# Optimization experiments

Hardware: AMD Instinct MI355X
Metric: run time of the kernel (lower is better)

Reference implementation:

```python
import jax, jax.numpy as jnp
import numpy as np


def setup_inputs() -> dict:
    key = jax.random.key(0)
    B, L, D, N = 2, 2048, 1024, 16
    ks = jax.random.split(key, 8)
    s = 1.0 / np.sqrt(D)
    # S4D-real init for A_log, matching the module
    A_log = jnp.log(jnp.broadcast_to(jnp.arange(1, N + 1, dtype=jnp.float32), (D, N)))
    return {
        "x": jax.random.normal(ks[0], (B, L, D), jnp.float32),
        "Wz": jax.random.normal(ks[1], (D, D), jnp.float32) * s,
        "bz": jnp.zeros((D,), jnp.float32),
        "Wx": jax.random.normal(ks[2], (D, D), jnp.float32) * s,
        "bx": jnp.zeros((D,), jnp.float32),
        "WB": jax.random.normal(ks[3], (D, N), jnp.float32) * s,
        "bB": jnp.zeros((N,), jnp.float32),
        "WC": jax.random.normal(ks[4], (D, N), jnp.float32) * s,
        "bC": jnp.zeros((N,), jnp.float32),
        "Wdt": jax.random.normal(ks[5], (D, D), jnp.float32) * s,
        "bdt": jnp.zeros((D,), jnp.float32),
        "A_log": A_log,
        "Wout": jax.random.normal(ks[6], (D, D), jnp.float32) * s,
        "bout": jnp.zeros((D,), jnp.float32),
    }


def reference(x, Wz, bz, Wx, bx, WB, bB, WC, bC, Wdt, bdt, A_log, Wout, bout):
    B, L, D = x.shape
    N = A_log.shape[1]

    # input-dependent projections
    z = jax.nn.sigmoid(x @ Wz + bz)            # (B,L,D) gate
    x_ssm = x @ Wx + bx                        # (B,L,D)
    Bm = x @ WB + bB                           # (B,L,N)
    C = x @ WC + bC                            # (B,L,N)
    dt = jax.nn.softplus(x @ Wdt + bdt)        # (B,L,D)

    A = -jnp.exp(A_log)                        # (D,N)
    A_bar = jnp.exp(dt[..., None] * A)         # (B,L,D,N) discretized state matrix
    # x_db = x_ssm * (dt * B)  -> (B,L,D,N)
    x_db = x_ssm[..., None] * (dt[..., None] * Bm[..., None, :])

    # scan over time: move L to leading axis
    a_scan = jnp.transpose(A_bar, (1, 0, 2, 3))   # (L,B,D,N)
    x_scan = jnp.transpose(x_db, (1, 0, 2, 3))    # (L,B,D,N)
    c_scan = jnp.transpose(C, (1, 0, 2))          # (L,B,N)

    def ssm_step(h, inp):
        a_t, x_t, c_t = inp                       # (B,D,N),(B,D,N),(B,N)
        h_new = a_t * h + x_t
        y_t = jnp.einsum('bdn,bn->bd', h_new, c_t)
        return h_new, y_t

    h0 = jnp.zeros((B, D, N), x.dtype)
    _, y_ssm = jax.lax.scan(ssm_step, h0, (a_scan, x_scan, c_scan))
    y_ssm = jnp.transpose(y_ssm, (1, 0, 2))       # (B,L,D)

    y = y_ssm * z
    return y @ Wout + bout
```

## Files before the change

### kernel.cpp

```cpp
#include <hip/hip_runtime.h>
#include <math.h>

#define CHUNKS 64
#define LCH    32

#define GBM 128
#define GBN 128
#define GBK 32
#define ATILE (GBM * GBK)
#define BTILE (GBN * GBK)

typedef __attribute__((ext_vector_type(8))) short bf16x8;
typedef __attribute__((ext_vector_type(4))) float f32x4;
typedef __attribute__((ext_vector_type(8))) unsigned short us8;
typedef __attribute__((ext_vector_type(4))) unsigned short us4;

typedef __attribute__((address_space(1))) const unsigned int gu32;
typedef __attribute__((address_space(3))) unsigned int lu32;

__device__ __forceinline__ void gload16(const unsigned short* g, unsigned short* l) {
    __builtin_amdgcn_global_load_lds((gu32*)g, (lu32*)l, 16, 0, 0);
}

__device__ __forceinline__ unsigned short f2bf(float f) {
    unsigned int u = __float_as_uint(f);
    unsigned int r = (u + 0x7FFFu + ((u >> 16) & 1u)) >> 16;
    return (unsigned short)r;
}
__device__ __forceinline__ float bf2f(unsigned short u) {
    return __uint_as_float((unsigned)u << 16);
}

__global__ __launch_bounds__(256) void transpose4_bf16(
    const float* __restrict__ W0, const float* __restrict__ W1,
    const float* __restrict__ W2, const float* __restrict__ W3,
    unsigned short* __restrict__ T0, unsigned short* __restrict__ T1,
    unsigned short* __restrict__ T2, unsigned short* __restrict__ T3, int D)
{
    const float* W = (blockIdx.z == 0) ? W0 : (blockIdx.z == 1) ? W1
                   : (blockIdx.z == 2) ? W2 : W3;
    unsigned short* Wt = (blockIdx.z == 0) ? T0 : (blockIdx.z == 1) ? T1
                       : (blockIdx.z == 2) ? T2 : T3;

    __shared__ float Ls[64][65];
    const int n0 = blockIdx.x * 64;
    const int k0 = blockIdx.y * 64;
    const int tx = threadIdx.x;

#pragma unroll
    for (int i = 0; i < 4; i++) {
        int idx = tx + i * 256;
        int kr = idx >> 4;
        int ng = idx & 15;
        float4 v = *(const float4*)&W[(size_t)(k0 + kr) * D + n0 + ng * 4];
        Ls[kr][ng * 4 + 0] = v.x;
        Ls[kr][ng * 4 + 1] = v.y;
        Ls[kr][ng * 4 + 2] = v.z;
        Ls[kr][ng * 4 + 3] = v.w;
    }
    __syncthreads();
#pragma unroll
    for (int i = 0; i < 4; i++) {
        int idx = tx + i * 256;
        int nr = idx >> 4;
        int kg = idx & 15;
        us4 u;
#pragma unroll
        for (int j = 0; j < 4; j++) u[j] = f2bf(Ls[kg * 4 + j][nr]);
        *(us4*)&Wt[(size_t)(n0 + nr) * D + k0 + kg * 4] = u;
    }
}

__device__ __forceinline__ void stage_tile(
    const unsigned short* __restrict__ A, const unsigned short* __restrict__ B,
    unsigned short* As, unsigned short* Bs,
    int brow, int bcol, int K, int k0, int wave, int srow, int sq)
{
    gload16(&A[(size_t)(brow + wave * 32      + srow) * K + k0 + sq],
            &As[(wave * 32) * GBK]);
    gload16(&A[(size_t)(brow + wave * 32 + 16 + srow) * K + k0 + sq],
            &As[(wave * 32 + 16) * GBK]);
    gload16(&B[(size_t)(bcol + wave * 32      + srow) * K + k0 + sq],
            &Bs[(wave * 32) * GBK]);
    gload16(&B[(size_t)(bcol + wave * 32 + 16 + srow) * K + k0 + sq],
            &Bs[(wave * 32 + 16) * GBK]);
}

__device__ __forceinline__ void gemm_core(
    const unsigned short* __restrict__ A, const unsigned short* __restrict__ B,
    unsigned short* As, unsigned short* Bs,
    int brow, int bcol, int K, f32x4 acc[4][4],
    int wave, int lane, int wr, int wc, int lrow, int lk)
{
    const int srow = lane >> 2;
    const int sq   = ((lane & 3) ^ ((lane >> 3) & 3)) * 8;

#pragma unroll
    for (int m = 0; m < 4; m++)
#pragma unroll
        for (int n = 0; n < 4; n++) acc[m][n] = (f32x4)(0.f);

    const int nk = K / GBK;
    stage_tile(A, B, As,         Bs,         brow, bcol, K, 0,   wave, srow, sq);
    stage_tile(A, B, As + ATILE, Bs + BTILE, brow, bcol, K, GBK, wave, srow, sq);

    int cur = 0;
    int nxt = 2;
    for (int kt = 0; kt < nk; ++kt) {
        if (kt + 2 < nk) {
            stage_tile(A, B, As + nxt * ATILE, Bs + nxt * BTILE,
                       brow, bcol, K, (kt + 2) * GBK, wave, srow, sq);
            asm volatile("s_waitcnt vmcnt(8)" ::: "memory");
        } else if (kt + 1 < nk) {
            asm volatile("s_waitcnt vmcnt(4)" ::: "memory");
        } else {
            asm volatile("s_waitcnt vmcnt(0)" ::: "memory");
        }
        __builtin_amdgcn_s_barrier();

        const unsigned short* as = As + cur * ATILE;
        const unsigned short* bs = Bs + cur * BTILE;

        bf16x8 av[4], bv[4];
#pragma unroll
        for (int m = 0; m < 4; m++) {
            int row = wr * 64 + m * 16 + lrow;
            av[m] = *(const bf16x8*)&as[row * GBK + ((lk ^ ((row >> 1) & 3)) * 8)];
        }
#pragma unroll
        for (int n = 0; n < 4; n++) {
            int row = wc * 64 + n * 16 + lrow;
            bv[n] = *(const bf16x8*)&bs[row * GBK + ((lk ^ ((row >> 1) & 3)) * 8)];
        }
#pragma unroll
        for (int m = 0; m < 4; m++)
#pragma unroll
            for (int n = 0; n < 4; n++)
                acc[m][n] = __builtin_amdgcn_mfma_f32_16x16x32_bf16(
                    av[m], bv[n], acc[m][n], 0, 0, 0);

        asm volatile("s_waitcnt lgkmcnt(0)" ::: "memory");
        __builtin_amdgcn_s_barrier();
        cur = (cur == 2) ? 0 : cur + 1;
        nxt = (nxt == 2) ? 0 : nxt + 1;
    }
}

__global__ __launch_bounds__(256) void proj3_gemm(
    const unsigned short* __restrict__ A,
    const unsigned short* __restrict__ W0, const unsigned short* __restrict__ W1,
    const unsigned short* __restrict__ W2,
    const float* __restrict__ b0, const float* __restrict__ b1,
    const float* __restrict__ b2,
    unsigned short* __restrict__ o0, unsigned short* __restrict__ o1,
    unsigned short* __restrict__ o2,
    int K, int Nc)
{
    __shared__ unsigned short As[3 * ATILE];
    __shared__ unsigned short Bs[3 * BTILE];

    const int bid = blockIdx.x;
    const int idx = bid >> 3;
    const int by  = (bid & 7) * 4 + idx / 24;
    const int bx  = idx % 24;

    const int widx = bx >> 3;
    const unsigned short* B = (widx == 0) ? W0 : (widx == 1) ? W1 : W2;
    const float* bias = (widx == 0) ? b0 : (widx == 1) ? b1 : b2;
    unsigned short* out = (widx == 0) ? o0 : (widx == 1) ? o1 : o2;

    const int tx = threadIdx.x;
    const int wave = tx >> 6;
    const int lane = tx & 63;
    const int wr = wave >> 1, wc = wave & 1;
    const int lrow = lane & 15, lk = lane >> 4;
    const int brow = by * GBM;
    const int bcol = (bx & 7) * GBN;

    f32x4 acc[4][4];
    gemm_core(A, B, As, Bs, brow, bcol, K, acc, wave, lane, wr, wc, lrow, lk);

#pragma unroll
    for (int n = 0; n < 4; n++) {
        int col = bcol + wc * 64 + n * 16 + lrow;
        float bval = bias[col];
#pragma unroll
        for (int m = 0; m < 4; m++) {
#pragma unroll
            for (int r = 0; r < 4; r++) {
                int row = brow + wr * 64 + m * 16 + lk * 4 + r;
                float v = acc[m][n][r] + bval;
                if (widx == 0) v = 1.f / (1.f + __expf(-v));
                else if (widx == 2) v = (v > 20.f) ? v : log1pf(__expf(v));
                out[(size_t)row * Nc + col] = f2bf(v);
            }
        }
    }
}

__global__ __launch_bounds__(256) void gemm_bt(
    const unsigned short* __restrict__ A, const unsigned short* __restrict__ B,
    const float* __restrict__ bias, float* __restrict__ out, int K, int ldo)
{
    __shared__ unsigned short As[3 * ATILE];
    __shared__ unsigned short Bs[3 * BTILE];

    const int bid = blockIdx.x;
    const int idx = bid >> 3;
    const int by  = (bid & 7) * 4 + idx / 8;
    const int bx  = idx % 8;

    const int tx = threadIdx.x;
    const int wave = tx >> 6;
    const int lane = tx & 63;
    const int wr = wave >> 1, wc = wave & 1;
    const int lrow = lane & 15, lk = lane >> 4;
    const int brow = by * GBM;
    const int bcol = bx * GBN;

    f32x4 acc[4][4];
    gemm_core(A, B, As, Bs, brow, bcol, K, acc, wave, lane, wr, wc, lrow, lk);

#pragma unroll
    for (int n = 0; n < 4; n++) {
        int col = bcol + wc * 64 + n * 16 + lrow;
        float bval = bias[col];
#pragma unroll
        for (int m = 0; m < 4; m++) {
#pragma unroll
            for (int r = 0; r < 4; r++) {
                int row = brow + wr * 64 + m * 16 + lk * 4 + r;
                out[(size_t)row * ldo + col] = acc[m][n][r] + bval;
            }
        }
    }
}

__global__ __launch_bounds__(256) void bc_proj(
    const float* __restrict__ x,
    const float* __restrict__ WB, const float* __restrict__ bB,
    const float* __restrict__ WC, const float* __restrict__ bC,
    float* __restrict__ BC, unsigned short* __restrict__ xbf, int K, int M)
{
    __shared__ unsigned short Wl[32 * 1024];

    const int tx = threadIdx.x;

#pragma unroll
    for (int i = 0; i < 16; i++) {
        int e = tx + i * 256;
        int k = e >> 2;
        int n0 = (e & 3) * 4;
        float4 v = ((const float4*)WB)[e];
        float vv[4] = {v.x, v.y, v.z, v.w};
#pragma unroll
        for (int j = 0; j < 4; j++) {
            int n = n0 + j;
            Wl[n * 1024 + (((k & ~7) ^ ((n & 15) << 3)) | (k & 7))] = f2bf(vv[j]);
        }
    }
#pragma unroll
    for (int i = 0; i < 16; i++) {
        int e = tx + i * 256;
        int k = e >> 2;
        int n0 = (e & 3) * 4;
        float4 v = ((const float4*)WC)[e];
        float vv[4] = {v.x, v.y, v.z, v.w};
#pragma unroll
        for (int j = 0; j < 4; j++) {
            int n = 16 + n0 + j;
            Wl[n * 1024 + (((k & ~7) ^ ((n & 15) << 3)) | (k & 7))] = f2bf(vv[j]);
        }
    }

#pragma unroll
    for (int i = 0; i < 4; i++) {
        int e = tx + i * 256;
        int rr = e >> 7;
        int cc = (e & 127) * 8;
        const float* src = &x[(size_t)(blockIdx.x * 8 + rr) * K + cc];
        float4 a = *(const float4*)src;
        float4 b = *(const float4*)(src + 4);
        us8 u;
        u[0] = f2bf(a.x); u[1] = f2bf(a.y); u[2] = f2bf(a.z); u[3] = f2bf(a.w);
        u[4] = f2bf(b.x); u[5] = f2bf(b.y); u[6] = f2bf(b.z); u[7] = f2bf(b.w);
        *(us8*)&xbf[(size_t)(blockIdx.x * 8 + rr) * K + cc] = u;
    }
    __syncthreads();

    const int n = tx & 31;
    const int r = tx >> 5;
    const int row = blockIdx.x * 8 + r;

    const unsigned short* wrow = &Wl[n * 1024];
    const int sw = (n & 15) << 3;
    const float* xrow = &x[(size_t)row * K];

    float acc = 0.f;
    for (int kb = 0; kb < K; kb += 8) {
        us8 w8 = *(const us8*)&wrow[kb ^ sw];
        float4 xa = *(const float4*)&xrow[kb];
        float4 xb = *(const float4*)&xrow[kb + 4];
        float xv[8] = {xa.x, xa.y, xa.z, xa.w, xb.x, xb.y, xb.z, xb.w};
#pragma unroll
        for (int j = 0; j < 8; j++) {
            acc = fmaf(xv[j], __uint_as_float((unsigned)(unsigned short)w8[j] << 16), acc);
        }
    }

    float bias = (n < 16) ? bB[n] : bC[n - 16];
    BC[(size_t)row * 32 + n] = acc + bias;
}

__global__ __launch_bounds__(256) void scan_phase1(
    const unsigned short* __restrict__ xs, const unsigned short* __restrict__ dt,
    const float* __restrict__ BC, const float* __restrict__ A_log,
    float* __restrict__ P, float* __restrict__ Hl, int L, int D, int M)
{
    const int tx = threadIdx.x;
    const int d  = blockIdx.x * 256 + tx;
    const int c  = blockIdx.y;
    const int b  = blockIdx.z;
    const int m0 = b * L + c * LCH;

    __shared__ float bcs[LCH][32];
    {
        int row = tx >> 3, col = (tx & 7) * 4;
        *(f32x4*)&bcs[row][col] = *(const f32x4*)&BC[(size_t)(m0 + row) * 32 + col];
    }
    __syncthreads();

    float Av[16];
#pragma unroll
    for (int i = 0; i < 4; i++) {
        f32x4 a4 = *(const f32x4*)&A_log[d * 16 + i * 4];
#pragma unroll
        for (int j = 0; j < 4; j++) Av[i * 4 + j] = -__expf(a4[j]);
    }

    float h[16];
#pragma unroll
    for (int n = 0; n < 16; n++) h[n] = 0.f;
    float dts = 0.f;

    const size_t base = (size_t)m0 * D + d;
    float dtv = bf2f(dt[base]), xv = bf2f(xs[base]);
    for (int t = 0; t < LCH; t++) {
        float dtn = 0.f, xvn = 0.f;
        if (t + 1 < LCH) {
            dtn = bf2f(dt[base + (size_t)(t + 1) * D]);
            xvn = bf2f(xs[base + (size_t)(t + 1) * D]);
        }
        float xdt = xv * dtv;
        dts += dtv;
        f32x4 bm[4];
#pragma unroll
        for (int i = 0; i < 4; i++) bm[i] = *(const f32x4*)&bcs[t][i * 4];
#pragma unroll
        for (int n = 0; n < 16; n++) {
            float a = __expf(dtv * Av[n]);
            h[n] = fmaf(a, h[n], xdt * bm[n >> 2][n & 3]);
        }
        dtv = dtn; xv = xvn;
    }

    size_t idx = (((size_t)b * D + d) * CHUNKS + c) * 16;
#pragma unroll
    for (int i = 0; i < 4; i++) {
        f32x4 p4, h4;
#pragma unroll
        for (int j = 0; j < 4; j++) {
            p4[j] = __expf(Av[i * 4 + j] * dts);
            h4[j] = h[i * 4 + j];
        }
        *(f32x4*)&P[idx + i * 4]  = p4;
        *(f32x4*)&Hl[idx + i * 4] = h4;
    }
}

__global__ __launch_bounds__(256) void scan_phase2(
    const float* __restrict__ P, float* __restrict__ Hl, int D, int N)
{
    const int tid = blockIdx.x * 256 + threadIdx.x;
    const int n = tid & 15;
    const int dd = (tid >> 4) & 1023;
    const int b = tid >> 14;

    size_t base = (((size_t)b * D + dd) * CHUNKS) * 16 + n;
    float run = 0.f;
#pragma unroll 4
    for (int c = 0; c < CHUNKS; c++) {
        float p   = P[base + (size_t)c * 16];
        float tmp = Hl[base + (size_t)c * 16];
        Hl[base + (size_t)c * 16] = run;
        run = fmaf(p, run, tmp);
    }
}

__global__ __launch_bounds__(256) void scan_phase3(
    const unsigned short* __restrict__ xs, const unsigned short* __restrict__ dt,
    const float* __restrict__ BC, const unsigned short* __restrict__ z,
    const float* __restrict__ A_log, const float* __restrict__ Hin,
    unsigned short* __restrict__ ybf, int L, int D, int M)
{
    const int tx = threadIdx.x;
    const int d  = blockIdx.x * 256 + tx;
    const int c  = blockIdx.y;
    const int b  = blockIdx.z;
    const int m0 = b * L + c * LCH;

    __shared__ float bcs[LCH][32];
    {
        int row = tx >> 3, col = (tx & 7) * 4;
        *(f32x4*)&bcs[row][col] = *(const f32x4*)&BC[(size_t)(m0 + row) * 32 + col];
    }
    __syncthreads();

    float Av[16];
#pragma unroll
    for (int i = 0; i < 4; i++) {
        f32x4 a4 = *(const f32x4*)&A_log[d * 16 + i * 4];
#pragma unroll
        for (int j = 0; j < 4; j++) Av[i * 4 + j] = -__expf(a4[j]);
    }

    float h[16];
    {
        size_t hidx = (((size_t)b * D + d) * CHUNKS + c) * 16;
#pragma unroll
        for (int i = 0; i < 4; i++) {
            f32x4 h4 = *(const f32x4*)&Hin[hidx + i * 4];
#pragma unroll
            for (int j = 0; j < 4; j++) h[i * 4 + j] = h4[j];
        }
    }

    const size_t base = (size_t)m0 * D + d;
    float dtv = bf2f(dt[base]), xv = bf2f(xs[base]), zv = bf2f(z[base]);
    for (int t = 0; t < LCH; t++) {
        float dtn = 0.f, xvn = 0.f, zvn = 0.f;
        if (t + 1 < LCH) {
            dtn = bf2f(dt[base + (size_t)(t + 1) * D]);
            xvn = bf2f(xs[base + (size_t)(t + 1) * D]);
            zvn = bf2f(z[base + (size_t)(t + 1) * D]);
        }
        float xdt = xv * dtv;
        f32x4 bm[4], cm[4];
#pragma unroll
        for (int i = 0; i < 4; i++) {
            bm[i] = *(const f32x4*)&bcs[t][i * 4];
            cm[i] = *(const f32x4*)&bcs[t][16 + i * 4];
        }
        float y = 0.f;
#pragma unroll
        for (int n = 0; n < 16; n++) {
            float a = __expf(dtv * Av[n]);
            h[n] = fmaf(a, h[n], xdt * bm[n >> 2][n & 3]);
            y = fmaf(h[n], cm[n >> 2][n & 3], y);
        }
        ybf[base + (size_t)t * D] = f2bf(y * zv);
        dtv = dtn; xv = xvn; zv = zvn;
    }
}

extern "C" void kernel_launch(void* const* d_in, const int* in_sizes, int n_in,
                              void* d_out, int out_size, void* d_ws, size_t ws_size,
                              hipStream_t stream) {
    const float* x     = (const float*)d_in[0];
    const float* Wz    = (const float*)d_in[1];
    const float* bz    = (const float*)d_in[2];
    const float* Wx    = (const float*)d_in[3];
    const float* bx    = (const float*)d_in[4];
    const float* WB    = (const float*)d_in[5];
    const float* bB    = (const float*)d_in[6];
    const float* WC    = (const float*)d_in[7];
    const float* bC    = (const float*)d_in[8];
    const float* Wdt   = (const float*)d_in[9];
    const float* bdt   = (const float*)d_in[10];
    const float* A_log = (const float*)d_in[11];
    const float* Wout  = (const float*)d_in[12];
    const float* bout  = (const float*)d_in[13];
    float* out = (float*)d_out;

    const int Bb = 2, L = 2048, D = 1024, N = 16;
    const int M = Bb * L;
    const size_t MD = (size_t)M * D;

    unsigned short* ws16 = (unsigned short*)d_ws;
    unsigned short* xsb  = ws16;
    unsigned short* dtb  = xsb + MD;
    float* BCb  = (float*)(dtb + MD);
    float* Pb   = BCb + (size_t)M * 32;
    float* Hlb  = Pb  + (size_t)Bb * D * CHUNKS * 16;
    unsigned short* xbf   = (unsigned short*)(Hlb + (size_t)Bb * D * CHUNKS * 16);
    unsigned short* Wzt   = xbf + MD;
    unsigned short* Wxt   = Wzt + (size_t)D * D;
    unsigned short* Wdtt  = Wxt + (size_t)D * D;
    unsigned short* Woutt = Wdtt + (size_t)D * D;
    unsigned short* zb = (unsigned short*)out;

    dim3 blk(256);
    dim3 gridT(D / 64, D / 64, 4);

    transpose4_bf16<<<gridT, blk, 0, stream>>>(Wz, Wx, Wdt, Wout,
                                               Wzt, Wxt, Wdtt, Woutt, D);
    bc_proj<<<dim3(M / 8), blk, 0, stream>>>(x, WB, bB, WC, bC, BCb, xbf, D, M);

    proj3_gemm<<<dim3(3 * (D / GBN) * (M / GBM)), blk, 0, stream>>>(
        xbf, Wzt, Wxt, Wdtt, bz, bx, bdt, zb, xsb, dtb, D, D);

    dim3 gridScan(D / 256, CHUNKS, Bb);
    scan_phase1<<<gridScan, blk, 0, stream>>>(xsb, dtb, BCb, A_log, Pb, Hlb, L, D, M);
    scan_phase2<<<dim3(Bb * D * N / 256), blk, 0, stream>>>(Pb, Hlb, D, N);
    scan_phase3<<<gridScan, blk, 0, stream>>>(xsb, dtb, BCb, zb, A_log, Hlb,
                                              xbf , L, D, M);

    gemm_bt<<<dim3((D / GBN) * (M / GBM)), blk, 0, stream>>>(xbf, Woutt, bout, out, D, D);
}
```

Before: 154.3 us.

## Replace triple-buffered K=32 GEMM pipeline with single-buffered K=64 tiles

Removes the three-stage LDS ring buffer and its prefetch and vmcnt bookkeeping from the shared bf16 GEMM core. It switches to one LDS buffer per operand with a K-tile of 64, a new XOR swizzle over 8 column groups, and two MFMA sub-steps per tile. This halves the number of barrier-separated iterations and shrinks LDS use, which may allow more blocks per CU. In exchange, global loads no longer overlap with the MFMA work, since each tile is loaded and then waited on before compute.

```diff
diff --git a/kernel.cpp b/kernel.cpp
--- a/kernel.cpp
+++ b/kernel.cpp
@@ -6,9 +6,8 @@
 
 #define GBM 128
 #define GBN 128
-#define GBK 32
-#define ATILE (GBM * GBK)
-#define BTILE (GBN * GBK)
+#define GBK 64
+#define KROW 64
 
 typedef __attribute__((ext_vector_type(8))) short bf16x8;
 typedef __attribute__((ext_vector_type(4))) float f32x4;
@@ -71,78 +70,51 @@
     }
 }
 
-__device__ __forceinline__ void stage_tile(
-    const unsigned short* __restrict__ A, const unsigned short* __restrict__ B,
-    unsigned short* As, unsigned short* Bs,
-    int brow, int bcol, int K, int k0, int wave, int srow, int sq)
-{
-    gload16(&A[(size_t)(brow + wave * 32      + srow) * K + k0 + sq],
-            &As[(wave * 32) * GBK]);
-    gload16(&A[(size_t)(brow + wave * 32 + 16 + srow) * K + k0 + sq],
-            &As[(wave * 32 + 16) * GBK]);
-    gload16(&B[(size_t)(bcol + wave * 32      + srow) * K + k0 + sq],
-            &Bs[(wave * 32) * GBK]);
-    gload16(&B[(size_t)(bcol + wave * 32 + 16 + srow) * K + k0 + sq],
-            &Bs[(wave * 32 + 16) * GBK]);
-}
-
 __device__ __forceinline__ void gemm_core(
     const unsigned short* __restrict__ A, const unsigned short* __restrict__ B,
     unsigned short* As, unsigned short* Bs,
     int brow, int bcol, int K, f32x4 acc[4][4],
     int wave, int lane, int wr, int wc, int lrow, int lk)
 {
-    const int srow = lane >> 2;
-    const int sq   = ((lane & 3) ^ ((lane >> 3) & 3)) * 8;
+    const int rg = lane >> 3;
+    const int sq = ((lane & 7) ^ rg) * 8;
+    const int swz = lrow & 7;
 
 #pragma unroll
     for (int m = 0; m < 4; m++)
 #pragma unroll
         for (int n = 0; n < 4; n++) acc[m][n] = (f32x4)(0.f);
 
-    const int nk = K / GBK;
-    stage_tile(A, B, As,         Bs,         brow, bcol, K, 0,   wave, srow, sq);
-    stage_tile(A, B, As + ATILE, Bs + BTILE, brow, bcol, K, GBK, wave, srow, sq);
-
-    int cur = 0;
-    int nxt = 2;
-    for (int kt = 0; kt < nk; ++kt) {
-        if (kt + 2 < nk) {
-            stage_tile(A, B, As + nxt * ATILE, Bs + nxt * BTILE,
-                       brow, bcol, K, (kt + 2) * GBK, wave, srow, sq);
-            asm volatile("s_waitcnt vmcnt(8)" ::: "memory");
-        } else if (kt + 1 < nk) {
-            asm volatile("s_waitcnt vmcnt(4)" ::: "memory");
-        } else {
-            asm volatile("s_waitcnt vmcnt(0)" ::: "memory");
-        }
-        __builtin_amdgcn_s_barrier();
-
-        const unsigned short* as = As + cur * ATILE;
-        const unsigned short* bs = Bs + cur * BTILE;
-
-        bf16x8 av[4], bv[4];
-#pragma unroll
-        for (int m = 0; m < 4; m++) {
-            int row = wr * 64 + m * 16 + lrow;
-            av[m] = *(const bf16x8*)&as[row * GBK + ((lk ^ ((row >> 1) & 3)) * 8)];
-        }
-#pragma unroll
-        for (int n = 0; n < 4; n++) {
-            int row = wc * 64 + n * 16 + lrow;
-            bv[n] = *(const bf16x8*)&bs[row * GBK + ((lk ^ ((row >> 1) & 3)) * 8)];
-        }
-#pragma unroll
-        for (int m = 0; m < 4; m++)
-#pragma unroll
-            for (int n = 0; n < 4; n++)
-                acc[m][n] = __builtin_amdgcn_mfma_f32_16x16x32_bf16(
-                    av[m], bv[n], acc[m][n], 0, 0, 0);
-
-        asm volatile("s_waitcnt lgkmcnt(0)" ::: "memory");
-        __builtin_amdgcn_s_barrier();
-        cur = (cur == 2) ? 0 : cur + 1;
-        nxt = (nxt == 2) ? 0 : nxt + 1;
+    for (int k0 = 0; k0 < K; k0 += GBK) {
+#pragma unroll
+        for (int i = 0; i < 4; i++) {
+            int r0 = wave * 32 + i * 8;
+            gload16(&A[(size_t)(brow + r0 + rg) * K + k0 + sq], &As[r0 * KROW]);
+            gload16(&B[(size_t)(bcol + r0 + rg) * K + k0 + sq], &Bs[r0 * KROW]);
+        }
+        __syncthreads();
+
+#pragma unroll
+        for (int kk = 0; kk < 2; kk++) {
+            bf16x8 av[4], bv[4];
+#pragma unroll
+            for (int m = 0; m < 4; m++) {
+                int row = wr * 64 + m * 16 + lrow;
+                av[m] = *(const bf16x8*)&As[row * KROW + (((kk * 4 + lk) ^ swz) * 8)];
+            }
+#pragma unroll
+            for (int n = 0; n < 4; n++) {
+                int row = wc * 64 + n * 16 + lrow;
+                bv[n] = *(const bf16x8*)&Bs[row * KROW + (((kk * 4 + lk) ^ swz) * 8)];
+            }
+#pragma unroll
+            for (int m = 0; m < 4; m++)
+#pragma unroll
+                for (int n = 0; n < 4; n++)
+                    acc[m][n] = __builtin_amdgcn_mfma_f32_16x16x32_bf16(
+                        av[m], bv[n], acc[m][n], 0, 0, 0);
+        }
+        __syncthreads();
     }
 }
 
@@ -156,8 +128,8 @@
     unsigned short* __restrict__ o2,
     int K, int Nc)
 {
-    __shared__ unsigned short As[3 * ATILE];
-    __shared__ unsigned short Bs[3 * BTILE];
+    __shared__ unsigned short As[GBM * GBK];
+    __shared__ unsigned short Bs[GBN * GBK];
 
     const int bid = blockIdx.x;
     const int idx = bid >> 3;
@@ -202,8 +174,8 @@
     const unsigned short* __restrict__ A, const unsigned short* __restrict__ B,
     const float* __restrict__ bias, float* __restrict__ out, int K, int ldo)
 {
-    __shared__ unsigned short As[3 * ATILE];
-    __shared__ unsigned short Bs[3 * BTILE];
+    __shared__ unsigned short As[GBM * GBK];
+    __shared__ unsigned short Bs[GBN * GBK];
 
     const int bid = blockIdx.x;
     const int idx = bid >> 3;
```

Result: slower. 179.7 us (+16.4%).

## Fuse three scan phases into one cooperative kernel with grid syncs

Applied to the files above, without the earlier changes.

Merges the chunked scan's local pass, cross-chunk prefix pass, and output pass into a single cooperatively launched kernel of 512 blocks, separated by grid-wide barriers. This removes two kernel launches and lets the output pass reuse the shared-memory B/C tile and the A values already computed. Separately, the B/C projection kernel now handles 16 rows per block instead of 8, which halves how often the weight tile is staged in shared memory. The cost is two grid barriers, and the middle phase leaves most blocks idle.

```diff
diff --git a/kernel.cpp b/kernel.cpp
--- a/kernel.cpp
+++ b/kernel.cpp
@@ -1,5 +1,8 @@
 #include <hip/hip_runtime.h>
+#include <hip/hip_cooperative_groups.h>
 #include <math.h>
+
+namespace cg = cooperative_groups;
 
 #define CHUNKS 64
 #define LCH    32
@@ -274,54 +277,64 @@
     }
 
 #pragma unroll
-    for (int i = 0; i < 4; i++) {
+    for (int i = 0; i < 8; i++) {
         int e = tx + i * 256;
         int rr = e >> 7;
         int cc = (e & 127) * 8;
-        const float* src = &x[(size_t)(blockIdx.x * 8 + rr) * K + cc];
+        const float* src = &x[(size_t)(blockIdx.x * 16 + rr) * K + cc];
         float4 a = *(const float4*)src;
         float4 b = *(const float4*)(src + 4);
         us8 u;
         u[0] = f2bf(a.x); u[1] = f2bf(a.y); u[2] = f2bf(a.z); u[3] = f2bf(a.w);
         u[4] = f2bf(b.x); u[5] = f2bf(b.y); u[6] = f2bf(b.z); u[7] = f2bf(b.w);
-        *(us8*)&xbf[(size_t)(blockIdx.x * 8 + rr) * K + cc] = u;
+        *(us8*)&xbf[(size_t)(blockIdx.x * 16 + rr) * K + cc] = u;
     }
     __syncthreads();
 
     const int n = tx & 31;
     const int r = tx >> 5;
-    const int row = blockIdx.x * 8 + r;
-
-    const unsigned short* wrow = &Wl[n * 1024];
-    const int sw = (n & 15) << 3;
-    const float* xrow = &x[(size_t)row * K];
-
-    float acc = 0.f;
-    for (int kb = 0; kb < K; kb += 8) {
-        us8 w8 = *(const us8*)&wrow[kb ^ sw];
-        float4 xa = *(const float4*)&xrow[kb];
-        float4 xb = *(const float4*)&xrow[kb + 4];
-        float xv[8] = {xa.x, xa.y, xa.z, xa.w, xb.x, xb.y, xb.z, xb.w};
-#pragma unroll
-        for (int j = 0; j < 8; j++) {
-            acc = fmaf(xv[j], __uint_as_float((unsigned)(unsigned short)w8[j] << 16), acc);
-        }
-    }
-
-    float bias = (n < 16) ? bB[n] : bC[n - 16];
-    BC[(size_t)row * 32 + n] = acc + bias;
-}
-
-__global__ __launch_bounds__(256) void scan_phase1(
+
+#pragma unroll
+    for (int rr4 = 0; rr4 < 2; rr4++) {
+        const int row = blockIdx.x * 16 + rr4 * 8 + r;
+
+        const unsigned short* wrow = &Wl[n * 1024];
+        const int sw = (n & 15) << 3;
+        const float* xrow = &x[(size_t)row * K];
+
+        float acc = 0.f;
+        for (int kb = 0; kb < K; kb += 8) {
+            us8 w8 = *(const us8*)&wrow[kb ^ sw];
+            float4 xa = *(const float4*)&xrow[kb];
+            float4 xb = *(const float4*)&xrow[kb + 4];
+            float xv[8] = {xa.x, xa.y, xa.z, xa.w, xb.x, xb.y, xb.z, xb.w};
+#pragma unroll
+            for (int j = 0; j < 8; j++) {
+                acc = fmaf(xv[j], __uint_as_float((unsigned)(unsigned short)w8[j] << 16), acc);
+            }
+        }
+
+        float bias = (n < 16) ? bB[n] : bC[n - 16];
+        BC[(size_t)row * 32 + n] = acc + bias;
+    }
+}
+
+__global__ __launch_bounds__(256) void scan_fused(
     const unsigned short* __restrict__ xs, const unsigned short* __restrict__ dt,
-    const float* __restrict__ BC, const float* __restrict__ A_log,
-    float* __restrict__ P, float* __restrict__ Hl, int L, int D, int M)
-{
-    const int tx = threadIdx.x;
-    const int d  = blockIdx.x * 256 + tx;
-    const int c  = blockIdx.y;
-    const int b  = blockIdx.z;
-    const int m0 = b * L + c * LCH;
+    const float* __restrict__ BC, const unsigned short* __restrict__ z,
+    const float* __restrict__ A_log,
+    float* __restrict__ P, float* __restrict__ Hl,
+    unsigned short* __restrict__ ybf, int L, int D, int M)
+{
+    cg::grid_group grid = cg::this_grid();
+
+    const int tx  = threadIdx.x;
+    const int bid = blockIdx.x;
+    const int dblk = bid & 3;
+    const int c    = (bid >> 2) & 63;
+    const int b    = bid >> 8;
+    const int d    = dblk * 256 + tx;
+    const int m0   = b * L + c * LCH;
 
     __shared__ float bcs[LCH][32];
     {
@@ -338,128 +351,104 @@
         for (int j = 0; j < 4; j++) Av[i * 4 + j] = -__expf(a4[j]);
     }
 
-    float h[16];
-#pragma unroll
-    for (int n = 0; n < 16; n++) h[n] = 0.f;
-    float dts = 0.f;
-
     const size_t base = (size_t)m0 * D + d;
-    float dtv = bf2f(dt[base]), xv = bf2f(xs[base]);
-    for (int t = 0; t < LCH; t++) {
-        float dtn = 0.f, xvn = 0.f;
-        if (t + 1 < LCH) {
-            dtn = bf2f(dt[base + (size_t)(t + 1) * D]);
-            xvn = bf2f(xs[base + (size_t)(t + 1) * D]);
-        }
-        float xdt = xv * dtv;
-        dts += dtv;
-        f32x4 bm[4];
-#pragma unroll
-        for (int i = 0; i < 4; i++) bm[i] = *(const f32x4*)&bcs[t][i * 4];
-#pragma unroll
-        for (int n = 0; n < 16; n++) {
-            float a = __expf(dtv * Av[n]);
-            h[n] = fmaf(a, h[n], xdt * bm[n >> 2][n & 3]);
-        }
-        dtv = dtn; xv = xvn;
-    }
-
-    size_t idx = (((size_t)b * D + d) * CHUNKS + c) * 16;
-#pragma unroll
-    for (int i = 0; i < 4; i++) {
-        f32x4 p4, h4;
-#pragma unroll
-        for (int j = 0; j < 4; j++) {
-            p4[j] = __expf(Av[i * 4 + j] * dts);
-            h4[j] = h[i * 4 + j];
-        }
-        *(f32x4*)&P[idx + i * 4]  = p4;
-        *(f32x4*)&Hl[idx + i * 4] = h4;
-    }
-}
-
-__global__ __launch_bounds__(256) void scan_phase2(
-    const float* __restrict__ P, float* __restrict__ Hl, int D, int N)
-{
-    const int tid = blockIdx.x * 256 + threadIdx.x;
-    const int n = tid & 15;
-    const int dd = (tid >> 4) & 1023;
-    const int b = tid >> 14;
-
-    size_t base = (((size_t)b * D + dd) * CHUNKS) * 16 + n;
-    float run = 0.f;
+    const size_t hidx = (((size_t)b * D + d) * CHUNKS + c) * 16;
+
+    {
+        float h[16];
+#pragma unroll
+        for (int n = 0; n < 16; n++) h[n] = 0.f;
+        float dts = 0.f;
+
+        float dtv = bf2f(dt[base]), xv = bf2f(xs[base]);
+        for (int t = 0; t < LCH; t++) {
+            float dtn = 0.f, xvn = 0.f;
+            if (t + 1 < LCH) {
+                dtn = bf2f(dt[base + (size_t)(t + 1) * D]);
+                xvn = bf2f(xs[base + (size_t)(t + 1) * D]);
+            }
+            float xdt = xv * dtv;
+            dts += dtv;
+            f32x4 bm[4];
+#pragma unroll
+            for (int i = 0; i < 4; i++) bm[i] = *(const f32x4*)&bcs[t][i * 4];
+#pragma unroll
+            for (int n = 0; n < 16; n++) {
+                float a = __expf(dtv * Av[n]);
+                h[n] = fmaf(a, h[n], xdt * bm[n >> 2][n & 3]);
+            }
+            dtv = dtn; xv = xvn;
+        }
+
+#pragma unroll
+        for (int i = 0; i < 4; i++) {
+            f32x4 p4, h4;
+#pragma unroll
+            for (int j = 0; j < 4; j++) {
+                p4[j] = __expf(Av[i * 4 + j] * dts);
+                h4[j] = h[i * 4 + j];
+            }
+            *(f32x4*)&P[hidx + i * 4]  = p4;
+            *(f32x4*)&Hl[hidx + i * 4] = h4;
+        }
+    }
+
+    grid.sync();
+
+    {
+        const int gtid = bid * 256 + tx;
+        if (gtid < 32768) {
+            const int n2 = gtid & 15;
+            const int dd = (gtid >> 4) & 1023;
+            const int b2 = gtid >> 14;
+            size_t base2 = (((size_t)b2 * D + dd) * CHUNKS) * 16 + n2;
+            float run = 0.f;
 #pragma unroll 4
-    for (int c = 0; c < CHUNKS; c++) {
-        float p   = P[base + (size_t)c * 16];
-        float tmp = Hl[base + (size_t)c * 16];
-        Hl[base + (size_t)c * 16] = run;
-        run = fmaf(p, run, tmp);
-    }
-}
-
-__global__ __launch_bounds__(256) void scan_phase3(
-    const unsigned short* __restrict__ xs, const unsigned short* __restrict__ dt,
-    const float* __restrict__ BC, const unsigned short* __restrict__ z,
-    const float* __restrict__ A_log, const float* __restrict__ Hin,
-    unsigned short* __restrict__ ybf, int L, int D, int M)
-{
-    const int tx = threadIdx.x;
-    const int d  = blockIdx.x * 256 + tx;
-    const int c  = blockIdx.y;
-    const int b  = blockIdx.z;
-    const int m0 = b * L + c * LCH;
-
-    __shared__ float bcs[LCH][32];
+            for (int cc = 0; cc < CHUNKS; cc++) {
+                float p   = P[base2 + (size_t)cc * 16];
+                float tmp = Hl[base2 + (size_t)cc * 16];
+                Hl[base2 + (size_t)cc * 16] = run;
+                run = fmaf(p, run, tmp);
+            }
+        }
+    }
+
+    grid.sync();
+
     {
-        int row = tx >> 3, col = (tx & 7) * 4;
-        *(f32x4*)&bcs[row][col] = *(const f32x4*)&BC[(size_t)(m0 + row) * 32 + col];
-    }
-    __syncthreads();
-
-    float Av[16];
-#pragma unroll
-    for (int i = 0; i < 4; i++) {
-        f32x4 a4 = *(const f32x4*)&A_log[d * 16 + i * 4];
-#pragma unroll
-        for (int j = 0; j < 4; j++) Av[i * 4 + j] = -__expf(a4[j]);
-    }
-
-    float h[16];
-    {
-        size_t hidx = (((size_t)b * D + d) * CHUNKS + c) * 16;
+        float h[16];
 #pragma unroll
         for (int i = 0; i < 4; i++) {
-            f32x4 h4 = *(const f32x4*)&Hin[hidx + i * 4];
+            f32x4 h4 = *(const f32x4*)&Hl[hidx + i * 4];
 #pragma unroll
             for (int j = 0; j < 4; j++) h[i * 4 + j] = h4[j];
         }
-    }
-
-    const size_t base = (size_t)m0 * D + d;
-    float dtv = bf2f(dt[base]), xv = bf2f(xs[base]), zv = bf2f(z[base]);
-    for (int t = 0; t < LCH; t++) {
-        float dtn = 0.f, xvn = 0.f, zvn = 0.f;
-        if (t + 1 < LCH) {
-            dtn = bf2f(dt[base + (size_t)(t + 1) * D]);
-            xvn = bf2f(xs[base + (size_t)(t + 1) * D]);
-            zvn = bf2f(z[base + (size_t)(t + 1) * D]);
-        }
-        float xdt = xv * dtv;
-        f32x4 bm[4], cm[4];
-#pragma unroll
-        for (int i = 0; i < 4; i++) {
-            bm[i] = *(const f32x4*)&bcs[t][i * 4];
-            cm[i] = *(const f32x4*)&bcs[t][16 + i * 4];
-        }
-        float y = 0.f;
-#pragma unroll
-        for (int n = 0; n < 16; n++) {
-            float a = __expf(dtv * Av[n]);
-            h[n] = fmaf(a, h[n], xdt * bm[n >> 2][n & 3]);
-            y = fmaf(h[n], cm[n >> 2][n & 3], y);
-        }
-        ybf[base + (size_t)t * D] = f2bf(y * zv);
-        dtv = dtn; xv = xvn; zv = zvn;
+
+        float dtv = bf2f(dt[base]), xv = bf2f(xs[base]), zv = bf2f(z[base]);
+        for (int t = 0; t < LCH; t++) {
+            float dtn = 0.f, xvn = 0.f, zvn = 0.f;
+            if (t + 1 < LCH) {
+                dtn = bf2f(dt[base + (size_t)(t + 1) * D]);
+                xvn = bf2f(xs[base + (size_t)(t + 1) * D]);
+                zvn = bf2f(z[base + (size_t)(t + 1) * D]);
+            }
+            float xdt = xv * dtv;
+            f32x4 bm[4], cm[4];
+#pragma unroll
+            for (int i = 0; i < 4; i++) {
+                bm[i] = *(const f32x4*)&bcs[t][i * 4];
+                cm[i] = *(const f32x4*)&bcs[t][16 + i * 4];
+            }
+            float y = 0.f;
+#pragma unroll
+            for (int n = 0; n < 16; n++) {
+                float a = __expf(dtv * Av[n]);
+                h[n] = fmaf(a, h[n], xdt * bm[n >> 2][n & 3]);
+                y = fmaf(h[n], cm[n >> 2][n & 3], y);
+            }
+            ybf[base + (size_t)t * D] = f2bf(y * zv);
+            dtv = dtn; xv = xvn; zv = zvn;
+        }
     }
 }
 
@@ -504,16 +493,25 @@
 
     transpose4_bf16<<<gridT, blk, 0, stream>>>(Wz, Wx, Wdt, Wout,
                                                Wzt, Wxt, Wdtt, Woutt, D);
-    bc_proj<<<dim3(M / 8), blk, 0, stream>>>(x, WB, bB, WC, bC, BCb, xbf, D, M);
+    bc_proj<<<dim3(M / 16), blk, 0, stream>>>(x, WB, bB, WC, bC, BCb, xbf, D, M);
 
     proj3_gemm<<<dim3(3 * (D / GBN) * (M / GBM)), blk, 0, stream>>>(
         xbf, Wzt, Wxt, Wdtt, bz, bx, bdt, zb, xsb, dtb, D, D);
 
-    dim3 gridScan(D / 256, CHUNKS, Bb);
-    scan_phase1<<<gridScan, blk, 0, stream>>>(xsb, dtb, BCb, A_log, Pb, Hlb, L, D, M);
-    scan_phase2<<<dim3(Bb * D * N / 256), blk, 0, stream>>>(Pb, Hlb, D, N);
-    scan_phase3<<<gridScan, blk, 0, stream>>>(xsb, dtb, BCb, zb, A_log, Hlb,
-                                              xbf , L, D, M);
+    {
+        const unsigned short* a_xs = xsb;
+        const unsigned short* a_dt = dtb;
+        const float* a_bc = BCb;
+        const unsigned short* a_z = zb;
+        const float* a_al = A_log;
+        float* a_p = Pb;
+        float* a_hl = Hlb;
+        unsigned short* a_y = xbf;
+        int a_L = L, a_D = D, a_M = M;
+        void* args[] = {&a_xs, &a_dt, &a_bc, &a_z, &a_al, &a_p, &a_hl, &a_y,
+                        &a_L, &a_D, &a_M};
+        hipLaunchCooperativeKernel((void*)scan_fused, dim3(512), blk, args, 0, stream);
+    }
 
     gemm_bt<<<dim3((D / GBN) * (M / GBM)), blk, 0, stream>>>(xbf, Woutt, bout, out, D, D);
 }
```

Measured after the change: 314.3 us. 104% more time.
